# Kernel optimization log

Measured on AMD Instinct MI355X. Metric: run time of the kernel, lower is better.

The kernel has to match this reference:

```python
import jax, jax.numpy as jnp
import numpy as np

D_IN = 1024
D_OUT = 1024
NUM_HEADS = 16
HEAD_DIM = D_OUT // NUM_HEADS


def setup_inputs() -> dict:
    key = jax.random.key(0)
    ks = jax.random.split(key, 6)
    B, T = 2, 2048
    x = jax.random.normal(ks[0], (B, T, D_IN), dtype=jnp.float32)
    s = 1.0 / np.sqrt(D_IN)
    Wq = jax.random.normal(ks[1], (D_IN, D_OUT), dtype=jnp.float32) * s
    Wk = jax.random.normal(ks[2], (D_IN, D_OUT), dtype=jnp.float32) * s
    Wv = jax.random.normal(ks[3], (D_IN, D_OUT), dtype=jnp.float32) * s
    Wo = jax.random.normal(ks[4], (D_OUT, D_OUT), dtype=jnp.float32) * (1.0 / np.sqrt(D_OUT))
    bo = jnp.zeros((D_OUT,), dtype=jnp.float32)
    return {"x": x, "Wq": Wq, "Wk": Wk, "Wv": Wv, "Wo": Wo, "bo": bo}


def reference(x, Wq, Wk, Wv, Wo, bo):
    B, T, _ = x.shape
    # project and split heads -> (B, H, T, Dh)
    def split(t):
        return t.reshape(B, T, NUM_HEADS, HEAD_DIM).transpose(0, 2, 1, 3)
    Q = split(x @ Wq)
    K = split(x @ Wk)
    V = split(x @ Wv)
    scale = HEAD_DIM ** -0.5
    scores = jnp.einsum('bhqd,bhkd->bhqk', Q, K) * scale  # (B,H,T,T)
    causal = jnp.triu(jnp.ones((T, T), dtype=bool), k=1)
    scores = jnp.where(causal, -jnp.inf, scores)
    weights = jax.nn.softmax(scores, axis=-1)
    ctx = jnp.einsum('bhqk,bhkd->bhqd', weights, V)  # (B,H,T,Dh)
    ctx = ctx.transpose(0, 2, 1, 3).reshape(B, T, D_OUT)
    return ctx @ Wo + bo
```

## Files before the change

kernel.cpp:

```cpp
#include <hip/hip_runtime.h>
#include <hip/hip_bf16.h>

#define NH   16
#define HD   64
#define BB   2
#define TT   2048
#define DIN  1024
#define DOUT 1024
#define MTOT (BB*TT)

#define QSCALE 0.18033688011112042f
#define MAXC   20.0f

typedef __hip_bfloat16 bf16;
typedef short bf16x8  __attribute__((ext_vector_type(8)));
typedef float f32x4   __attribute__((ext_vector_type(4)));
typedef float f32x16  __attribute__((ext_vector_type(16)));

__device__ __forceinline__ bf16 f2bf(float f){ return __float2bfloat16(f); }

__device__ __forceinline__ size_t frag_off(int r, int k){
    return (size_t)((r>>4)*32 + (k>>5))*512 + (size_t)(((r&15) + 16*((k>>3)&3))*8) + (k&7);
}
__device__ __forceinline__ size_t qk_off(int bh, int t, int d){
    return (size_t)bh*131072 + (size_t)(((t>>5)*4 + (d>>4))*512)
         + ((t&31) + 32*((d>>3)&1))*8 + (d&7);
}
__device__ __forceinline__ size_t v_off(int bh, int t, int d){
    return (size_t)bh*131072 + (size_t)((((t>>4)*2) + (d>>5))*512)
         + ((d&31) + 32*((t>>2)&1))*8 + ((t&3) + 4*((t>>3)&1));
}

__global__ void prep_all(const float* __restrict__ x,
                         const float* __restrict__ Wq, const float* __restrict__ Wk,
                         const float* __restrict__ Wv, const float* __restrict__ Wo,
                         bf16* __restrict__ Xf, bf16* __restrict__ Wf){
    __shared__ float tile[64][65];
    const int blk = blockIdx.x;
    if (blk < 4096){
        int i = blk*256 + threadIdx.x;
        float4 v = ((const float4*)x)[i];
        bf16 o[4] = {f2bf(v.x), f2bf(v.y), f2bf(v.z), f2bf(v.w)};
        int m = i >> 8, k = (i & 255) << 2;
        *(ushort4*)&Xf[frag_off(m, k)] = *(ushort4*)o;
        return;
    }
    const int wb = blk - 4096;
    const int n0 = (wb >> 4) * 64, k0 = (wb & 15) * 64;
    const float* W;
    switch (n0 >> 10){ case 0: W=Wq; break; case 1: W=Wk; break; case 2: W=Wv; break; default: W=Wo; }
    const int c0 = n0 & 1023;
    const int tr = threadIdx.x >> 6;
    const int tc = threadIdx.x & 63;
    #pragma unroll
    for (int it = 0; it < 16; it++){
        int k = k0 + it*4 + tr;
        tile[it*4 + tr][tc] = W[(size_t)k*DOUT + c0 + tc];
    }
    __syncthreads();
    #pragma unroll
    for (int it = 0; it < 4; it++){
        int n_loc = tc;
        int k_loc = ((tr*4) + it) * 4;
        bf16 o[4];
        #pragma unroll
        for (int j = 0; j < 4; j++) o[j] = f2bf(tile[k_loc + j][n_loc]);
        *(ushort4*)&Wf[frag_off(n0 + n_loc, k0 + k_loc)] = *(ushort4*)o;
    }
}

__launch_bounds__(256, 3)
__global__ void gemm_qkv(const bf16* __restrict__ Xf, const bf16* __restrict__ Wf,
                         bf16* __restrict__ Qf, bf16* __restrict__ Kf, bf16* __restrict__ Vf){
    const int blk = blockIdx.x;
    const int n0 = (blk % 48) * 64;
    const int m0 = (blk / 48) * 256;
    const int wave = threadIdx.x >> 6, lane = threadIdx.x & 63;
    const int quad = lane >> 4, l16 = lane & 15;
    const bf16* Ab = Xf + (size_t)((m0 >> 4) + wave*4)*32*512 + lane*8;
    const bf16* Bb = Wf + (size_t)(n0 >> 4)*32*512 + lane*8;

    bf16x8 af[2][4], bfr[2][4];
    #pragma unroll
    for (int s = 0; s < 2; s++){
        #pragma unroll
        for (int i = 0; i < 4; i++){
            af[s][i]  = *(const bf16x8*)(Ab + ((size_t)i*32 + s)*512);
            bfr[s][i] = *(const bf16x8*)(Bb + ((size_t)i*32 + s)*512);
        }
    }
    f32x4 acc[4][4] = {};
    for (int kt = 0; kt < 32; kt += 2){
        #pragma unroll
        for (int s = 0; s < 2; s++){
            #pragma unroll
            for (int mi = 0; mi < 4; mi++)
                #pragma unroll
                for (int ni = 0; ni < 4; ni++)
                    acc[mi][ni] = __builtin_amdgcn_mfma_f32_16x16x32_bf16(af[s][mi], bfr[s][ni], acc[mi][ni], 0, 0, 0);
            int kn = kt + 2 + s;
            if (kn < 32){
                #pragma unroll
                for (int i = 0; i < 4; i++){
                    af[s][i]  = *(const bf16x8*)(Ab + ((size_t)i*32 + kn)*512);
                    bfr[s][i] = *(const bf16x8*)(Bb + ((size_t)i*32 + kn)*512);
                }
            }
        }
    }
    #pragma unroll
    for (int mi = 0; mi < 4; mi++){
        #pragma unroll
        for (int ni = 0; ni < 4; ni++){
            int col = n0 + ni*16 + l16;
            int which = col >> 10;
            int c = col & 1023;
            int h = c >> 6, d = c & 63;
            int m_base = m0 + wave*64 + mi*16 + quad*4;
            int b = m_base >> 11, t0 = m_base & 2047;
            int bh = b*NH + h;
            if (which == 2){
                bf16 pk[4];
                #pragma unroll
                for (int r = 0; r < 4; r++) pk[r] = f2bf(acc[mi][ni][r]);
                *(ushort4*)&Vf[v_off(bh, t0, d)] = *(ushort4*)pk;
            } else if (which == 0){
                #pragma unroll
                for (int r = 0; r < 4; r++)
                    Qf[qk_off(bh, t0 + r, d)] = f2bf(acc[mi][ni][r] * QSCALE);
            } else {
                #pragma unroll
                for (int r = 0; r < 4; r++)
                    Kf[qk_off(bh, t0 + r, d)] = f2bf(acc[mi][ni][r]);
            }
        }
    }
}

__launch_bounds__(256, 4)
__global__ void attn(const bf16* __restrict__ Qf, const bf16* __restrict__ Kf,
                     const bf16* __restrict__ Vf, bf16* __restrict__ ctx){
    __shared__ float Lo[3*64*36];
    __shared__ float Ls[3*64];
    const int blk  = blockIdx.x;
    const int bh   = (blk & 7) + 8*((blk >> 3) & 3);
    const int qb   = 63 - (blk >> 5);
    const int wave = threadIdx.x >> 6, lane = threadIdx.x & 63;
    const int n    = qb + 1;
    const int tstart = (n*wave) >> 2;
    const int tend   = ((n*(wave+1)) >> 2) - 1;
    const int h32  = lane >> 5, l32 = lane & 31;
    const int b    = bh >> 4, head = bh & 15;
    const bf16* Qb = Qf + (size_t)bh*131072 + lane*8;
    const bf16* Kb = Kf + (size_t)bh*131072 + lane*8;
    const bf16* Vb = Vf + (size_t)bh*131072 + lane*8;

    bf16x8 qf[4];
    #pragma unroll
    for (int ks = 0; ks < 4; ks++)
        qf[ks] = *(const bf16x8*)(Qb + (qb*4 + ks)*512);

    bf16x8 kc[4], vc[4];
    #pragma unroll
    for (int i = 0; i < 4; i++){
        kc[i] = *(const bf16x8*)(Kb + (tstart*4 + i)*512);
        vc[i] = *(const bf16x8*)(Vb + (tstart*4 + i)*512);
    }

    f32x16 o0 = {}, o1 = {};
    float lsum = 0.f;

    for (int tb = tstart; tb <= tend; tb++){
        f32x16 s = {};
        #pragma unroll
        for (int ks = 0; ks < 4; ks++)
            s = __builtin_amdgcn_mfma_f32_32x32x16_bf16(kc[ks], qf[ks], s, 0, 0, 0);
        if (tb < tend){
            #pragma unroll
            for (int i = 0; i < 4; i++)
                kc[i] = *(const bf16x8*)(Kb + ((tb+1)*4 + i)*512);
        }
        if (tb == qb){
            #pragma unroll
            for (int r = 0; r < 16; r++){
                int trow = (r&3) + 8*(r>>2) + 4*h32;
                if (trow > l32) s[r] = -1e30f;
            }
        }
        float p[16];
        #pragma unroll
        for (int r = 0; r < 16; r++){
            p[r] = __builtin_amdgcn_exp2f(s[r] - MAXC);
            lsum += p[r];
        }
        #pragma unroll
        for (int ki = 0; ki < 2; ki++){
            bf16 pb[8];
            #pragma unroll
            for (int j = 0; j < 8; j++) pb[j] = f2bf(p[ki*8 + j]);
            bf16x8 pbv = *(bf16x8*)pb;
            o0 = __builtin_amdgcn_mfma_f32_32x32x16_bf16(vc[ki*2+0], pbv, o0, 0, 0, 0);
            o1 = __builtin_amdgcn_mfma_f32_32x32x16_bf16(vc[ki*2+1], pbv, o1, 0, 0, 0);
        }
        if (tb < tend){
            #pragma unroll
            for (int i = 0; i < 4; i++)
                vc[i] = *(const bf16x8*)(Vb + ((tb+1)*4 + i)*512);
        }
    }

    if (wave != 0){
        float* lo = &Lo[(wave-1)*2304 + lane*36];
        #pragma unroll
        for (int c = 0; c < 4; c++){
            f32x4 w4 = { o0[c*4+0], o0[c*4+1], o0[c*4+2], o0[c*4+3] };
            *(f32x4*)&lo[c*4] = w4;
        }
        #pragma unroll
        for (int c = 0; c < 4; c++){
            f32x4 w4 = { o1[c*4+0], o1[c*4+1], o1[c*4+2], o1[c*4+3] };
            *(f32x4*)&lo[16 + c*4] = w4;
        }
        Ls[(wave-1)*64 + lane] = lsum;
    }
    __syncthreads();
    if (wave == 0){
        float lc = lsum;
        #pragma unroll
        for (int w = 0; w < 3; w++){
            const float* lo = &Lo[w*2304 + lane*36];
            #pragma unroll
            for (int c = 0; c < 4; c++){
                f32x4 r4 = *(const f32x4*)&lo[c*4];
                #pragma unroll
                for (int i = 0; i < 4; i++) o0[c*4+i] += r4[i];
            }
            #pragma unroll
            for (int c = 0; c < 4; c++){
                f32x4 r4 = *(const f32x4*)&lo[16 + c*4];
                #pragma unroll
                for (int i = 0; i < 4; i++) o1[c*4+i] += r4[i];
            }
            lc += Ls[w*64 + lane];
        }
        float lq  = lc + __shfl_xor(lc, 32);
        float inv = 1.0f / lq;
        const int q = qb*32 + l32;
        const int mrow = b*TT + q;
        #pragma unroll
        for (int db = 0; db < 2; db++){
            #pragma unroll
            for (int rq = 0; rq < 4; rq++){
                bf16 pk[4];
                #pragma unroll
                for (int i = 0; i < 4; i++){
                    float ov = (db ? o1[rq*4 + i] : o0[rq*4 + i]) * inv;
                    pk[i] = f2bf(ov);
                }
                int ch = head*HD + db*32 + rq*8 + h32*4;
                *(ushort4*)&ctx[frag_off(mrow, ch)] = *(ushort4*)pk;
            }
        }
    }
}

__launch_bounds__(256, 2)
__global__ void gemm_out(const bf16* __restrict__ Cf, const bf16* __restrict__ Wf,
                         const float* __restrict__ bo, float* __restrict__ out){
    const int blk = blockIdx.x;
    const int n0 = (blk % 32) * 32;
    const int m0 = (blk / 32) * 256;
    const int wave = threadIdx.x >> 6, lane = threadIdx.x & 63;
    const int quad = lane >> 4, l16 = lane & 15;
    const bf16* Ab = Cf + (size_t)((m0 >> 4) + wave*4)*32*512 + lane*8;
    const bf16* Bb = Wf + (size_t)((3072 + n0) >> 4)*32*512 + lane*8;

    bf16x8 af[2][4], bfr[2][2];
    #pragma unroll
    for (int s = 0; s < 2; s++){
        #pragma unroll
        for (int i = 0; i < 4; i++) af[s][i]  = *(const bf16x8*)(Ab + ((size_t)i*32 + s)*512);
        #pragma unroll
        for (int i = 0; i < 2; i++) bfr[s][i] = *(const bf16x8*)(Bb + ((size_t)i*32 + s)*512);
    }
    f32x4 acc[4][2] = {};
    for (int kt = 0; kt < 32; kt += 2){
        #pragma unroll
        for (int s = 0; s < 2; s++){
            #pragma unroll
            for (int mi = 0; mi < 4; mi++)
                #pragma unroll
                for (int ni = 0; ni < 2; ni++)
                    acc[mi][ni] = __builtin_amdgcn_mfma_f32_16x16x32_bf16(af[s][mi], bfr[s][ni], acc[mi][ni], 0, 0, 0);
            int kn = kt + 2 + s;
            if (kn < 32){
                #pragma unroll
                for (int i = 0; i < 4; i++) af[s][i]  = *(const bf16x8*)(Ab + ((size_t)i*32 + kn)*512);
                #pragma unroll
                for (int i = 0; i < 2; i++) bfr[s][i] = *(const bf16x8*)(Bb + ((size_t)i*32 + kn)*512);
            }
        }
    }
    #pragma unroll
    for (int mi = 0; mi < 4; mi++){
        #pragma unroll
        for (int ni = 0; ni < 2; ni++){
            int nn = n0 + ni*16 + l16;
            float bias = bo[nn];
            #pragma unroll
            for (int r = 0; r < 4; r++){
                int m = m0 + wave*64 + mi*16 + quad*4 + r;
                out[(size_t)m*DOUT + nn] = acc[mi][ni][r] + bias;
            }
        }
    }
}

extern "C" void kernel_launch(void* const* d_in, const int* in_sizes, int n_in,
                              void* d_out, int out_size, void* d_ws, size_t ws_size,
                              hipStream_t stream){
    const float* x  = (const float*)d_in[0];
    const float* Wq = (const float*)d_in[1];
    const float* Wk = (const float*)d_in[2];
    const float* Wv = (const float*)d_in[3];
    const float* Wo = (const float*)d_in[4];
    const float* bo = (const float*)d_in[5];
    float* out = (float*)d_out;

    char* ws = (char*)d_ws;
    bf16* Xf  = (bf16*)(ws);
    bf16* Wf  = (bf16*)(ws + ((size_t)8  << 20));
    bf16* Qf  = (bf16*)(ws + ((size_t)16 << 20));
    bf16* Kf  = (bf16*)(ws + ((size_t)24 << 20));
    bf16* Vf  = (bf16*)(ws + ((size_t)32 << 20));
    bf16* Cf  = (bf16*)(ws + ((size_t)40 << 20));

    prep_all <<<dim3(5120), 256, 0, stream>>>(x, Wq, Wk, Wv, Wo, Xf, Wf);
    gemm_qkv <<<dim3(768),  256, 0, stream>>>(Xf, Wf, Qf, Kf, Vf);
    attn     <<<dim3(2048), 256, 0, stream>>>(Qf, Kf, Vf, Cf);
    gemm_out <<<dim3(512),  256, 0, stream>>>(Cf, Wf, bo, out);
}
```

Measured before the change: 180.9 us.

## Restructure attention work split, retile GEMMs, and vectorize prep conversion stores

The attention kernel drops the split of one query block's key range across four waves, which required an LDS reduction and barrier. Each wave now owns its own query block, with 512 blocks paired so long and short causal rows are interleaved. Both GEMMs move to 2x2 wave tiles (128x128 and 128x64 per block) to share A and B fragment loads across waves. The prep kernel writes 8-element bf16 vectors in fragment layout using fewer blocks. The new attention split can leave waves within a block unevenly loaded and gives fewer blocks overall, trading occupancy for less reduction overhead.

```diff
diff --git a/kernel.cpp b/kernel.cpp
--- a/kernel.cpp
+++ b/kernel.cpp
@@ -36,22 +36,28 @@
                          const float* __restrict__ Wv, const float* __restrict__ Wo,
                          bf16* __restrict__ Xf, bf16* __restrict__ Wf){
     __shared__ float tile[64][65];
-    const int blk = blockIdx.x;
-    if (blk < 4096){
-        int i = blk*256 + threadIdx.x;
-        float4 v = ((const float4*)x)[i];
-        bf16 o[4] = {f2bf(v.x), f2bf(v.y), f2bf(v.z), f2bf(v.w)};
-        int m = i >> 8, k = (i & 255) << 2;
-        *(ushort4*)&Xf[frag_off(m, k)] = *(ushort4*)o;
+    const int blk = blockIdx.x, tid = threadIdx.x;
+    if (blk < 256){
+        const int wave = tid >> 6, l = tid & 63;
+        const int m = blk*16 + (l & 15);
+        #pragma unroll
+        for (int i = 0; i < 8; i++){
+            int kg = wave + i*4;
+            int k  = kg*32 + 8*(l >> 4);
+            float4 a = *(const float4*)&x[(size_t)m*DIN + k];
+            float4 c = *(const float4*)&x[(size_t)m*DIN + k + 4];
+            bf16 o[8] = {f2bf(a.x),f2bf(a.y),f2bf(a.z),f2bf(a.w),
+                         f2bf(c.x),f2bf(c.y),f2bf(c.z),f2bf(c.w)};
+            *(bf16x8*)&Xf[(size_t)(blk*32 + kg)*512 + l*8] = *(bf16x8*)o;
+        }
         return;
     }
-    const int wb = blk - 4096;
+    const int wb = blk - 256;
     const int n0 = (wb >> 4) * 64, k0 = (wb & 15) * 64;
     const float* W;
     switch (n0 >> 10){ case 0: W=Wq; break; case 1: W=Wk; break; case 2: W=Wv; break; default: W=Wo; }
     const int c0 = n0 & 1023;
-    const int tr = threadIdx.x >> 6;
-    const int tc = threadIdx.x & 63;
+    const int tr = tid >> 6, tc = tid & 63;
     #pragma unroll
     for (int it = 0; it < 16; it++){
         int k = k0 + it*4 + tr;
@@ -59,13 +65,16 @@
     }
     __syncthreads();
     #pragma unroll
-    for (int it = 0; it < 4; it++){
-        int n_loc = tc;
-        int k_loc = ((tr*4) + it) * 4;
-        bf16 o[4];
-        #pragma unroll
-        for (int j = 0; j < 4; j++) o[j] = f2bf(tile[k_loc + j][n_loc]);
-        *(ushort4*)&Wf[frag_off(n0 + n_loc, k0 + k_loc)] = *(ushort4*)o;
+    for (int it = 0; it < 2; it++){
+        int u  = it*256 + tid;
+        int sg = u >> 6, l = u & 63;
+        int ng = sg >> 1, kg = sg & 1;
+        int nl = ng*16 + (l & 15);
+        int kl = kg*32 + 8*(l >> 4);
+        bf16 o[8];
+        #pragma unroll
+        for (int j = 0; j < 8; j++) o[j] = f2bf(tile[kl + j][nl]);
+        *(bf16x8*)&Wf[frag_off(n0 + nl, k0 + kl)] = *(bf16x8*)o;
     }
 }
 
@@ -73,12 +82,12 @@
 __global__ void gemm_qkv(const bf16* __restrict__ Xf, const bf16* __restrict__ Wf,
                          bf16* __restrict__ Qf, bf16* __restrict__ Kf, bf16* __restrict__ Vf){
     const int blk = blockIdx.x;
-    const int n0 = (blk % 48) * 64;
-    const int m0 = (blk / 48) * 256;
+    const int n0 = (blk % 24) * 128;
+    const int m0 = (blk / 24) * 128;
     const int wave = threadIdx.x >> 6, lane = threadIdx.x & 63;
     const int quad = lane >> 4, l16 = lane & 15;
-    const bf16* Ab = Xf + (size_t)((m0 >> 4) + wave*4)*32*512 + lane*8;
-    const bf16* Bb = Wf + (size_t)(n0 >> 4)*32*512 + lane*8;
+    const bf16* Ab = Xf + (size_t)((m0 >> 4) + (wave & 1)*4)*32*512 + lane*8;
+    const bf16* Bb = Wf + (size_t)((n0 >> 4) + (wave >> 1)*4)*32*512 + lane*8;
 
     bf16x8 af[2][4], bfr[2][4];
     #pragma unroll
@@ -112,11 +121,11 @@
     for (int mi = 0; mi < 4; mi++){
         #pragma unroll
         for (int ni = 0; ni < 4; ni++){
-            int col = n0 + ni*16 + l16;
+            int col = n0 + (wave >> 1)*64 + ni*16 + l16;
             int which = col >> 10;
             int c = col & 1023;
             int h = c >> 6, d = c & 63;
-            int m_base = m0 + wave*64 + mi*16 + quad*4;
+            int m_base = m0 + (wave & 1)*64 + mi*16 + quad*4;
             int b = m_base >> 11, t0 = m_base & 2047;
             int bh = b*NH + h;
             if (which == 2){
@@ -137,18 +146,14 @@
     }
 }
 
-__launch_bounds__(256, 4)
+__launch_bounds__(256, 2)
 __global__ void attn(const bf16* __restrict__ Qf, const bf16* __restrict__ Kf,
                      const bf16* __restrict__ Vf, bf16* __restrict__ ctx){
-    __shared__ float Lo[3*64*36];
-    __shared__ float Ls[3*64];
     const int blk  = blockIdx.x;
-    const int bh   = (blk & 7) + 8*((blk >> 3) & 3);
-    const int qb   = 63 - (blk >> 5);
+    const int bh   = blk & 31;
+    const int qg   = (blk < 256) ? (15 - (blk >> 5)) : ((blk >> 5) - 8);
     const int wave = threadIdx.x >> 6, lane = threadIdx.x & 63;
-    const int n    = qb + 1;
-    const int tstart = (n*wave) >> 2;
-    const int tend   = ((n*(wave+1)) >> 2) - 1;
+    const int qb   = qg*4 + wave;
     const int h32  = lane >> 5, l32 = lane & 31;
     const int b    = bh >> 4, head = bh & 15;
     const bf16* Qb = Qf + (size_t)bh*131072 + lane*8;
@@ -163,19 +168,19 @@
     bf16x8 kc[4], vc[4];
     #pragma unroll
     for (int i = 0; i < 4; i++){
-        kc[i] = *(const bf16x8*)(Kb + (tstart*4 + i)*512);
-        vc[i] = *(const bf16x8*)(Vb + (tstart*4 + i)*512);
+        kc[i] = *(const bf16x8*)(Kb + i*512);
+        vc[i] = *(const bf16x8*)(Vb + i*512);
     }
 
     f32x16 o0 = {}, o1 = {};
     float lsum = 0.f;
 
-    for (int tb = tstart; tb <= tend; tb++){
+    for (int tb = 0; tb <= qb; tb++){
         f32x16 s = {};
         #pragma unroll
         for (int ks = 0; ks < 4; ks++)
             s = __builtin_amdgcn_mfma_f32_32x32x16_bf16(kc[ks], qf[ks], s, 0, 0, 0);
-        if (tb < tend){
+        if (tb < qb){
             #pragma unroll
             for (int i = 0; i < 4; i++)
                 kc[i] = *(const bf16x8*)(Kb + ((tb+1)*4 + i)*512);
@@ -202,78 +207,41 @@
             o0 = __builtin_amdgcn_mfma_f32_32x32x16_bf16(vc[ki*2+0], pbv, o0, 0, 0, 0);
             o1 = __builtin_amdgcn_mfma_f32_32x32x16_bf16(vc[ki*2+1], pbv, o1, 0, 0, 0);
         }
-        if (tb < tend){
+        if (tb < qb){
             #pragma unroll
             for (int i = 0; i < 4; i++)
                 vc[i] = *(const bf16x8*)(Vb + ((tb+1)*4 + i)*512);
         }
     }
-
-    if (wave != 0){
-        float* lo = &Lo[(wave-1)*2304 + lane*36];
-        #pragma unroll
-        for (int c = 0; c < 4; c++){
-            f32x4 w4 = { o0[c*4+0], o0[c*4+1], o0[c*4+2], o0[c*4+3] };
-            *(f32x4*)&lo[c*4] = w4;
-        }
-        #pragma unroll
-        for (int c = 0; c < 4; c++){
-            f32x4 w4 = { o1[c*4+0], o1[c*4+1], o1[c*4+2], o1[c*4+3] };
-            *(f32x4*)&lo[16 + c*4] = w4;
-        }
-        Ls[(wave-1)*64 + lane] = lsum;
-    }
-    __syncthreads();
-    if (wave == 0){
-        float lc = lsum;
-        #pragma unroll
-        for (int w = 0; w < 3; w++){
-            const float* lo = &Lo[w*2304 + lane*36];
-            #pragma unroll
-            for (int c = 0; c < 4; c++){
-                f32x4 r4 = *(const f32x4*)&lo[c*4];
-                #pragma unroll
-                for (int i = 0; i < 4; i++) o0[c*4+i] += r4[i];
-            }
-            #pragma unroll
-            for (int c = 0; c < 4; c++){
-                f32x4 r4 = *(const f32x4*)&lo[16 + c*4];
-                #pragma unroll
-                for (int i = 0; i < 4; i++) o1[c*4+i] += r4[i];
-            }
-            lc += Ls[w*64 + lane];
-        }
-        float lq  = lc + __shfl_xor(lc, 32);
-        float inv = 1.0f / lq;
-        const int q = qb*32 + l32;
-        const int mrow = b*TT + q;
-        #pragma unroll
-        for (int db = 0; db < 2; db++){
-            #pragma unroll
-            for (int rq = 0; rq < 4; rq++){
-                bf16 pk[4];
-                #pragma unroll
-                for (int i = 0; i < 4; i++){
-                    float ov = (db ? o1[rq*4 + i] : o0[rq*4 + i]) * inv;
-                    pk[i] = f2bf(ov);
-                }
-                int ch = head*HD + db*32 + rq*8 + h32*4;
-                *(ushort4*)&ctx[frag_off(mrow, ch)] = *(ushort4*)pk;
-            }
-        }
-    }
-}
-
-__launch_bounds__(256, 2)
+    float lq  = lsum + __shfl_xor(lsum, 32);
+    float inv = 1.0f / lq;
+    const int mrow = b*TT + qb*32 + l32;
+    #pragma unroll
+    for (int db = 0; db < 2; db++){
+        #pragma unroll
+        for (int rq = 0; rq < 4; rq++){
+            bf16 pk[4];
+            #pragma unroll
+            for (int i = 0; i < 4; i++){
+                float ov = (db ? o1[rq*4 + i] : o0[rq*4 + i]) * inv;
+                pk[i] = f2bf(ov);
+            }
+            int ch = head*HD + db*32 + rq*8 + h32*4;
+            *(ushort4*)&ctx[frag_off(mrow, ch)] = *(ushort4*)pk;
+        }
+    }
+}
+
+__launch_bounds__(256, 3)
 __global__ void gemm_out(const bf16* __restrict__ Cf, const bf16* __restrict__ Wf,
                          const float* __restrict__ bo, float* __restrict__ out){
     const int blk = blockIdx.x;
-    const int n0 = (blk % 32) * 32;
-    const int m0 = (blk / 32) * 256;
+    const int n0 = (blk & 15) * 64;
+    const int m0 = (blk >> 4) * 128;
     const int wave = threadIdx.x >> 6, lane = threadIdx.x & 63;
     const int quad = lane >> 4, l16 = lane & 15;
-    const bf16* Ab = Cf + (size_t)((m0 >> 4) + wave*4)*32*512 + lane*8;
-    const bf16* Bb = Wf + (size_t)((3072 + n0) >> 4)*32*512 + lane*8;
+    const bf16* Ab = Cf + (size_t)((m0 >> 4) + (wave & 1)*4)*32*512 + lane*8;
+    const bf16* Bb = Wf + (size_t)(((3072 + n0) >> 4) + (wave >> 1)*2)*32*512 + lane*8;
 
     bf16x8 af[2][4], bfr[2][2];
     #pragma unroll
@@ -305,11 +273,11 @@
     for (int mi = 0; mi < 4; mi++){
         #pragma unroll
         for (int ni = 0; ni < 2; ni++){
-            int nn = n0 + ni*16 + l16;
+            int nn = n0 + (wave >> 1)*32 + ni*16 + l16;
             float bias = bo[nn];
             #pragma unroll
             for (int r = 0; r < 4; r++){
-                int m = m0 + wave*64 + mi*16 + quad*4 + r;
+                int m = m0 + (wave & 1)*64 + mi*16 + quad*4 + r;
                 out[(size_t)m*DOUT + nn] = acc[mi][ni][r] + bias;
             }
         }
@@ -335,8 +303,8 @@
     bf16* Vf  = (bf16*)(ws + ((size_t)32 << 20));
     bf16* Cf  = (bf16*)(ws + ((size_t)40 << 20));
 
-    prep_all <<<dim3(5120), 256, 0, stream>>>(x, Wq, Wk, Wv, Wo, Xf, Wf);
+    prep_all <<<dim3(1280), 256, 0, stream>>>(x, Wq, Wk, Wv, Wo, Xf, Wf);
     gemm_qkv <<<dim3(768),  256, 0, stream>>>(Xf, Wf, Qf, Kf, Vf);
-    attn     <<<dim3(2048), 256, 0, stream>>>(Qf, Kf, Vf, Cf);
+    attn     <<<dim3(512),  256, 0, stream>>>(Qf, Kf, Vf, Cf);
     gemm_out <<<dim3(512),  256, 0, stream>>>(Cf, Wf, bo, out);
 }
```

Result: no change. 179.1 us (-1.0%).
